# Optimization experiments

Hardware: AMD Instinct MI355X
Metric: run time of the kernel (lower is better)

Reference implementation:

```python
import jax, jax.numpy as jnp
import numpy as np

DIMS = 1024
HEAD = 16
HEAD_DIM = DIMS // HEAD
MAX_ITERS = 3
THRESH = 0.01   # torch uses self.threshold.item() -> plain float, no grad
FACTOR = 0.1    # torch uses self.factor.item()
EPS = 1e-5


def _ln(x, w):
    # LayerNorm(bias=False): (x-mean)/sqrt(var+eps) * w
    m = jnp.mean(x, axis=-1, keepdims=True)
    xc = x - m
    v = jnp.mean(xc * xc, axis=-1, keepdims=True)
    return xc * jax.lax.rsqrt(v + EPS) * w


def _focus(xw, Wq, bq, Wk, Wv, bv, Wo, bo, lna_w, lnb_w,
           lq_w, lq_b, lk_w, lk_b, lv_w, lv_b):
    # xw: [B, S, DIMS]. NOTE: in the torch code xa is effectively ignored inside
    # create_qkv (k/v are computed from x due to the `xa is not None` branch bug),
    # so each window is pure self-attention on the query window.
    B, S, D = xw.shape
    xn = _ln(xw, lna_w)
    scale = HEAD_DIM ** -0.25
    q = (xn @ Wq.T + bq) * scale
    k = (xn @ Wk.T) * scale          # k Linear has no bias
    v = xn @ Wv.T + bv

    def shp(t):
        return t.reshape(B, S, HEAD, HEAD_DIM).transpose(0, 2, 1, 3)  # [B,h,S,d]

    q, k, v = shp(q), shp(k), shp(v)
    q = _ln(q, lnb_w)
    k = _ln(k, lnb_w)

    causal = jnp.tril(jnp.ones((S, S), dtype=bool))
    neg = jnp.finfo(jnp.float32).min
    inv_sqrt_d = 1.0 / np.sqrt(HEAD_DIM).astype(np.float32)

    q_cur = q
    prev = jnp.zeros_like(q)
    attn_out = jnp.zeros_like(q)
    done = jnp.array(False)

    # eff_span == S here (span_len >= win_size, ctx % win_size == 0), so the
    # [:eff_span] slices in torch are no-ops. Unrolled loop with where-gating
    # reproduces the data-dependent early exit and stays reverse-differentiable.
    for it in range(MAX_ITERS):
        qp = _ln(q_cur @ lq_w.T + lq_b, lnb_w)
        kp = _ln(k @ lk_w.T + lk_b, lnb_w)
        vp = v @ lv_w.T + lv_b
        s = jnp.einsum('bhqd,bhkd->bhqk', qp, kp) * inv_sqrt_d
        s = jnp.where(causal, s, neg)
        a = jax.nn.softmax(s, axis=-1)
        o = jnp.einsum('bhqk,bhkd->bhqd', a, vp)
        # torch: permute(0,2,1,3).flatten(2) -> [B,S,h*d], then (buggy) raw
        # view(B, HEAD, S, HEAD_DIM) with NO transpose; out_proj is NOT applied
        # in this branch. Reproduced faithfully.
        iter_out = (o.transpose(0, 2, 1, 3)
                     .reshape(B, S, HEAD * HEAD_DIM)
                     .reshape(B, HEAD, S, HEAD_DIM))
        diff = jnp.mean(jnp.abs(iter_out - prev))
        conv = jnp.logical_and(diff < THRESH + FACTOR * diff, it > 0)
        attn_out = jnp.where(done, attn_out, iter_out)
        upd = jnp.logical_or(done, conv)
        q_cur = jnp.where(upd, q_cur, q_cur + iter_out)
        prev = jnp.where(upd, prev, iter_out)
        done = upd

    out = attn_out.transpose(0, 2, 1, 3).reshape(B, S, D)
    return out @ Wo.T + bo


def setup_inputs() -> dict:
    key = jax.random.key(0)
    ks = jax.random.split(key, 10)

    def w(k, shape, s=0.02):
        return jax.random.normal(k, shape, dtype=jnp.float32) * s

    return {
        'x': jax.random.normal(ks[0], (4, 4096, DIMS), dtype=jnp.float32),
        'Wq': w(ks[1], (DIMS, DIMS)), 'bq': jnp.zeros((DIMS,), jnp.float32),
        'Wk': w(ks[2], (DIMS, DIMS)),
        'Wv': w(ks[3], (DIMS, DIMS)), 'bv': jnp.zeros((DIMS,), jnp.float32),
        'Wo': w(ks[4], (DIMS, DIMS)), 'bo': jnp.zeros((DIMS,), jnp.float32),
        'lna_w': jnp.ones((DIMS,), jnp.float32),
        'lnb_w': jnp.ones((HEAD_DIM,), jnp.float32),
        'lq_w': w(ks[5], (HEAD_DIM, HEAD_DIM), 0.1), 'lq_b': jnp.zeros((HEAD_DIM,), jnp.float32),
        'lk_w': w(ks[6], (HEAD_DIM, HEAD_DIM), 0.1), 'lk_b': jnp.zeros((HEAD_DIM,), jnp.float32),
        'lv_w': w(ks[7], (HEAD_DIM, HEAD_DIM), 0.1), 'lv_b': jnp.zeros((HEAD_DIM,), jnp.float32),
        'win_size': 512,
        'span_len': 1024,
    }


def reference(x, Wq, bq, Wk, Wv, bv, Wo, bo, lna_w, lnb_w,
              lq_w, lq_b, lk_w, lk_b, lv_w, lv_b, win_size, span_len):
    # span_len only influences eff_span in torch; with span_len >= win_size it
    # has no effect on the math (k/v come from the query window due to the bug).
    b, ctx, dims = x.shape
    nwin = ctx // win_size  # ctx chosen divisible by win_size
    xw = x.reshape(b, nwin, win_size, dims).transpose(1, 0, 2, 3)  # [nwin,B,W,D]
    f = lambda xx: _focus(xx, Wq, bq, Wk, Wv, bv, Wo, bo, lna_w, lnb_w,
                          lq_w, lq_b, lk_w, lk_b, lv_w, lv_b)
    out = jax.vmap(f)(xw)  # per-window convergence test, matching torch
    return out.transpose(1, 0, 2, 3).reshape(b, ctx, dims)
```

## Files before the change

kernel.cpp:

```cpp
#include <hip/hip_runtime.h>
#include <math.h>

#define DIMS   1024
#define NHEAD  16
#define HD     64
#define WIN    512
#define CTX    4096
#define NBATCH 4
#define NROWS  (NBATCH*CTX)
#define NUNITS (NROWS*NHEAD)
#define LNEPS  1e-5f
#define FIXSCALE 16777216.0

typedef __attribute__((ext_vector_type(8))) short bf16x8;
typedef __attribute__((ext_vector_type(4))) float f32x4;

__device__ __forceinline__ float4 ld4(const float* p) { return *reinterpret_cast<const float4*>(p); }
__device__ __forceinline__ void st4(float* p, float4 v) { *reinterpret_cast<float4*>(p) = v; }

__device__ __forceinline__ float wave_sum64(float v) {
#pragma unroll
    for (int off = 32; off; off >>= 1) v += __shfl_xor(v, off, 64);
    return v;
}
__device__ __forceinline__ float grp16_sum(float v) {
    v += __shfl_xor(v, 1, 64);
    v += __shfl_xor(v, 2, 64);
    v += __shfl_xor(v, 4, 64);
    v += __shfl_xor(v, 8, 64);
    return v;
}

__device__ __forceinline__ unsigned bf16_rn_bits(float x) {
    unsigned u = __float_as_uint(x);
    return (u + 0x7fffu + ((u >> 16) & 1u)) >> 16;
}
__device__ __forceinline__ unsigned pack_hl(float x) {
    unsigned h = bf16_rn_bits(x);
    float hf = __uint_as_float(h << 16);
    unsigned l = bf16_rn_bits(x - hf);
    return (h << 16) | (l & 0xffffu);
}

__device__ __forceinline__ unsigned cvtpk_bf16(float a, float b) {
    unsigned r;
    asm volatile("v_cvt_pk_bf16_f32 %0, %1, %2" : "=v"(r) : "v"(a), "v"(b));
    return r;
}
__device__ __forceinline__ void split_pair(float a, float b, unsigned& hw, unsigned& lw) {
    hw = cvtpk_bf16(a, b);
    float ha = __uint_as_float(hw << 16);
    float hb = __uint_as_float(hw & 0xffff0000u);
    lw = cvtpk_bf16(a - ha, b - hb);
}

__device__ __forceinline__ int swzo(int row, int kbyte) {
    return ((row << 7) + kbyte) ^ ((row & 7) << 4);
}

__global__ __launch_bounds__(256)
void ln1024_pack_kernel(const float* __restrict__ x, const float* __restrict__ w,
                        unsigned* __restrict__ outp) {
    int r = blockIdx.x;
    int tid = threadIdx.x;
    const float* xr = x + (size_t)r * DIMS;
    float4 v = ld4(xr + (tid << 2));
    __shared__ float red[8];
    float s = wave_sum64(v.x + v.y + v.z + v.w);
    int wv = tid >> 6, lane = tid & 63;
    if (lane == 0) red[wv] = s;
    __syncthreads();
    float mean = (red[0] + red[1] + red[2] + red[3]) * (1.0f / DIMS);
    float dx = v.x - mean, dy = v.y - mean, dz = v.z - mean, dw = v.w - mean;
    float ss = wave_sum64(dx*dx + dy*dy + dz*dz + dw*dw);
    if (lane == 0) red[4 + wv] = ss;
    __syncthreads();
    float inv = rsqrtf((red[4] + red[5] + red[6] + red[7]) * (1.0f / DIMS) + LNEPS);
    float4 wv4 = ld4(w + (tid << 2));
    uint4 pk;
    pk.x = pack_hl(dx * inv * wv4.x);
    pk.y = pack_hl(dy * inv * wv4.y);
    pk.z = pack_hl(dz * inv * wv4.z);
    pk.w = pack_hl(dw * inv * wv4.w);
    *reinterpret_cast<uint4*>(outp + (size_t)r * DIMS + (tid << 2)) = pk;
}

template<int DO_HLN>
__global__ __launch_bounds__(256, 2)
void gemm_hl_kernel(const unsigned* __restrict__ Ahl, const float* __restrict__ W,
                    const float* __restrict__ bias, float* __restrict__ Cm,
                    float alpha, int has_bias, const float* __restrict__ lnw) {
    __shared__ short Ah[128 * 64], Al[128 * 64], Wh[128 * 64], Wl[128 * 64];
    int tid = threadIdx.x;
    int wid = tid >> 6, lane = tid & 63;
    int wm = (wid >> 1) << 6, wn = (wid & 1) << 6;
    int g4 = lane >> 4, l16 = lane & 15;
    int m0 = blockIdx.x << 7, n0 = blockIdx.y << 7;

    f32x4 acc[4][4] = {};

    int orow[4], okb[4];
#pragma unroll
    for (int j = 0; j < 4; ++j) {
        int oc = tid + (j << 8);
        orow[j] = oc >> 3;
        okb[j] = (oc & 7) << 4;
    }

    for (int k0 = 0; k0 < 1024; k0 += 64) {
        uint4 a0[4], a1[4];
        float4 w0[4], w1[4];
#pragma unroll
        for (int j = 0; j < 4; ++j) {
            const unsigned* ap = Ahl + (size_t)(m0 + orow[j]) * 1024 + k0 + (okb[j] >> 1);
            a0[j] = *reinterpret_cast<const uint4*>(ap);
            a1[j] = *reinterpret_cast<const uint4*>(ap + 4);
            const float* wp = W + (size_t)(n0 + orow[j]) * 1024 + k0 + (okb[j] >> 1);
            w0[j] = *reinterpret_cast<const float4*>(wp);
            w1[j] = *reinterpret_cast<const float4*>(wp + 4);
        }
        __syncthreads();
#pragma unroll
        for (int j = 0; j < 4; ++j) {
            int off = swzo(orow[j], okb[j]);
            uint4 hi, lo;
            hi.x = __byte_perm(a0[j].x, a0[j].y, 0x7632);
            hi.y = __byte_perm(a0[j].z, a0[j].w, 0x7632);
            hi.z = __byte_perm(a1[j].x, a1[j].y, 0x7632);
            hi.w = __byte_perm(a1[j].z, a1[j].w, 0x7632);
            lo.x = __byte_perm(a0[j].x, a0[j].y, 0x5410);
            lo.y = __byte_perm(a0[j].z, a0[j].w, 0x5410);
            lo.z = __byte_perm(a1[j].x, a1[j].y, 0x5410);
            lo.w = __byte_perm(a1[j].z, a1[j].w, 0x5410);
            *reinterpret_cast<uint4*>(reinterpret_cast<char*>(Ah) + off) = hi;
            *reinterpret_cast<uint4*>(reinterpret_cast<char*>(Al) + off) = lo;

            float xs[8];
            *reinterpret_cast<float4*>(&xs[0]) = w0[j];
            *reinterpret_cast<float4*>(&xs[4]) = w1[j];
            uint4 hw4, lw4;
            unsigned* hwp = &hw4.x;
            unsigned* lwp = &lw4.x;
#pragma unroll
            for (int p = 0; p < 4; ++p) {
                unsigned u0 = __float_as_uint(xs[2*p]);
                unsigned u1 = __float_as_uint(xs[2*p + 1]);
                unsigned h0 = (u0 + 0x8000u) >> 16;
                unsigned h1 = (u1 + 0x8000u) >> 16;
                float l0 = xs[2*p]     - __uint_as_float(h0 << 16);
                float l1 = xs[2*p + 1] - __uint_as_float(h1 << 16);
                unsigned lb0 = (__float_as_uint(l0) + 0x8000u) >> 16;
                unsigned lb1 = (__float_as_uint(l1) + 0x8000u) >> 16;
                hwp[p] = h0 | (h1 << 16);
                lwp[p] = lb0 | (lb1 << 16);
            }
            *reinterpret_cast<uint4*>(reinterpret_cast<char*>(Wh) + off) = hw4;
            *reinterpret_cast<uint4*>(reinterpret_cast<char*>(Wl) + off) = lw4;
        }
        __syncthreads();

#pragma unroll
        for (int kk = 0; kk < 2; ++kk) {
            bf16x8 afh[4], afl[4], wfh[4], wfl[4];
#pragma unroll
            for (int mt = 0; mt < 4; ++mt) {
                int row = wm + (mt << 4) + l16;
                int off = ((row << 7) + (kk << 6) + (g4 << 4)) ^ ((row & 7) << 4);
                afh[mt] = *reinterpret_cast<const bf16x8*>(reinterpret_cast<const char*>(Ah) + off);
                afl[mt] = *reinterpret_cast<const bf16x8*>(reinterpret_cast<const char*>(Al) + off);
            }
#pragma unroll
            for (int nt = 0; nt < 4; ++nt) {
                int row = wn + (nt << 4) + l16;
                int off = ((row << 7) + (kk << 6) + (g4 << 4)) ^ ((row & 7) << 4);
                wfh[nt] = *reinterpret_cast<const bf16x8*>(reinterpret_cast<const char*>(Wh) + off);
                wfl[nt] = *reinterpret_cast<const bf16x8*>(reinterpret_cast<const char*>(Wl) + off);
            }
#pragma unroll
            for (int mt = 0; mt < 4; ++mt)
#pragma unroll
                for (int nt = 0; nt < 4; ++nt) {
                    acc[mt][nt] = __builtin_amdgcn_mfma_f32_16x16x32_bf16(afh[mt], wfh[nt], acc[mt][nt], 0, 0, 0);
                    acc[mt][nt] = __builtin_amdgcn_mfma_f32_16x16x32_bf16(afl[mt], wfh[nt], acc[mt][nt], 0, 0, 0);
                    acc[mt][nt] = __builtin_amdgcn_mfma_f32_16x16x32_bf16(afh[mt], wfl[nt], acc[mt][nt], 0, 0, 0);
                }
        }
    }

    if (DO_HLN) {
        float bb[4];
#pragma unroll
        for (int nt = 0; nt < 4; ++nt)
            bb[nt] = has_bias ? bias[n0 + wn + (nt << 4) + l16] : 0.0f;
        float lw4[4];
#pragma unroll
        for (int nt = 0; nt < 4; ++nt) lw4[nt] = lnw[(nt << 4) + l16];
#pragma unroll
        for (int mt = 0; mt < 4; ++mt)
#pragma unroll
            for (int r = 0; r < 4; ++r) {
                float v[4];
                float s1 = 0.0f;
#pragma unroll
                for (int nt = 0; nt < 4; ++nt) {
                    v[nt] = alpha * (acc[mt][nt][r] + bb[nt]);
                    s1 += v[nt];
                }
                s1 = grp16_sum(s1);
                float mean = s1 * (1.0f / 64.0f);
                float s2 = 0.0f;
#pragma unroll
                for (int nt = 0; nt < 4; ++nt) { v[nt] -= mean; s2 += v[nt] * v[nt]; }
                s2 = grp16_sum(s2);
                float inv = rsqrtf(s2 * (1.0f / 64.0f) + LNEPS);
                int row = m0 + wm + (mt << 4) + (g4 << 2) + r;
#pragma unroll
                for (int nt = 0; nt < 4; ++nt)
                    Cm[(size_t)row * DIMS + n0 + wn + (nt << 4) + l16] = v[nt] * inv * lw4[nt];
            }
    } else {
#pragma unroll
        for (int mt = 0; mt < 4; ++mt)
#pragma unroll
            for (int nt = 0; nt < 4; ++nt) {
                int col = n0 + wn + (nt << 4) + l16;
                float bb = has_bias ? bias[col] : 0.0f;
#pragma unroll
                for (int r = 0; r < 4; ++r) {
                    int row = m0 + wm + (mt << 4) + (g4 << 2) + r;
                    Cm[(size_t)row * DIMS + col] = alpha * (acc[mt][nt][r] + bb);
                }
            }
    }
}

__global__ __launch_bounds__(256)
void proj64_khl_kernel(const float* __restrict__ inp, const float* __restrict__ W,
                       const float* __restrict__ Wb, const float* __restrict__ lnw,
                       unsigned* __restrict__ plane) {
    int u0 = blockIdx.x << 6;
    __shared__ float As[64][68];
    __shared__ float Bs[64][68];
    int tid = threadIdx.x;
    for (int e = tid; e < 4096; e += 256) Bs[e & 63][e >> 6] = W[e];
    for (int e = tid; e < 1024; e += 256) {
        int row = e >> 4;
        int col = (e & 15) << 2;
        float4 v = ld4(inp + ((size_t)(u0 + row) << 6) + col);
        As[col + 0][row] = v.x; As[col + 1][row] = v.y;
        As[col + 2][row] = v.z; As[col + 3][row] = v.w;
    }
    __syncthreads();
    int tm = tid >> 4, tn = tid & 15;
    float acc[4][4] = {};
#pragma unroll
    for (int k = 0; k < 64; ++k) {
        float4 av = ld4(&As[k][tm << 2]);
        float4 bv = ld4(&Bs[k][tn << 2]);
        float aa[4] = {av.x, av.y, av.z, av.w};
        float bb[4] = {bv.x, bv.y, bv.z, bv.w};
#pragma unroll
        for (int mm = 0; mm < 4; ++mm)
#pragma unroll
            for (int nn = 0; nn < 4; ++nn)
                acc[mm][nn] = fmaf(aa[mm], bb[nn], acc[mm][nn]);
    }
    float bb4[4] = {Wb[(tn << 2) + 0], Wb[(tn << 2) + 1], Wb[(tn << 2) + 2], Wb[(tn << 2) + 3]};
    float lw4[4] = {lnw[(tn << 2) + 0], lnw[(tn << 2) + 1], lnw[(tn << 2) + 2], lnw[(tn << 2) + 3]};
#pragma unroll
    for (int mm = 0; mm < 4; ++mm) {
        float o0 = acc[mm][0] + bb4[0], o1 = acc[mm][1] + bb4[1];
        float o2 = acc[mm][2] + bb4[2], o3 = acc[mm][3] + bb4[3];
        float mean = grp16_sum(o0 + o1 + o2 + o3) * (1.0f / 64.0f);
        float d0 = o0 - mean, d1 = o1 - mean, d2 = o2 - mean, d3 = o3 - mean;
        float var = grp16_sum(d0*d0 + d1*d1 + d2*d2 + d3*d3) * (1.0f / 64.0f);
        float inv = rsqrtf(var + LNEPS);
        o0 = d0 * inv * lw4[0]; o1 = d1 * inv * lw4[1];
        o2 = d2 * inv * lw4[2]; o3 = d3 * inv * lw4[3];
        int u_p = u0 + (tm << 2) + mm;
        int r = u_p >> 4, h = u_p & 15;
        int s = r & 511;
        int ua = ((r >> 9) << 4) + h;
        size_t punit = (size_t)ua * 512 + s;
        uint4 pk;
        pk.x = pack_hl(o0); pk.y = pack_hl(o1); pk.z = pack_hl(o2); pk.w = pack_hl(o3);
        *reinterpret_cast<uint4*>(plane + (punit << 6) + (tn << 2)) = pk;
    }
}

__global__ __launch_bounds__(256)
void proj64_vthl_kernel(const float* __restrict__ inp, const float* __restrict__ W,
                        const float* __restrict__ Wb, unsigned* __restrict__ plane) {
    int u0 = blockIdx.x << 6;
    __shared__ float As[64][68];
    __shared__ float Bs[64][68];
    int tid = threadIdx.x;
    for (int e = tid; e < 4096; e += 256) Bs[e & 63][e >> 6] = W[e];
    for (int e = tid; e < 1024; e += 256) {
        int row = e >> 4;
        int col = (e & 15) << 2;
        float4 v = ld4(inp + ((size_t)(u0 + row) << 6) + col);
        As[col + 0][row] = v.x; As[col + 1][row] = v.y;
        As[col + 2][row] = v.z; As[col + 3][row] = v.w;
    }
    __syncthreads();
    int tm = tid >> 4, tn = tid & 15;
    float acc[4][4] = {};
#pragma unroll
    for (int k = 0; k < 64; ++k) {
        float4 av = ld4(&As[k][tm << 2]);
        float4 bv = ld4(&Bs[k][tn << 2]);
        float aa[4] = {av.x, av.y, av.z, av.w};
        float bb[4] = {bv.x, bv.y, bv.z, bv.w};
#pragma unroll
        for (int mm = 0; mm < 4; ++mm)
#pragma unroll
            for (int nn = 0; nn < 4; ++nn)
                acc[mm][nn] = fmaf(aa[mm], bb[nn], acc[mm][nn]);
    }
    float bb4[4] = {Wb[(tn << 2) + 0], Wb[(tn << 2) + 1], Wb[(tn << 2) + 2], Wb[(tn << 2) + 3]};
#pragma unroll
    for (int mm = 0; mm < 4; ++mm) {
        int u_p = u0 + (tm << 2) + mm;
        int r = u_p >> 4, h = u_p & 15;
        int s = r & 511;
        int ua = ((r >> 9) << 4) + h;
        size_t base = ((size_t)(ua * 8 + (s >> 6)) << 12) + (s & 63);
#pragma unroll
        for (int nn = 0; nn < 4; ++nn) {
            int d = (tn << 2) + nn;
            plane[base + ((size_t)d << 6)] = pack_hl(acc[mm][nn] + bb4[nn]);
        }
    }
}

template<int DIFF, int USE_CONV>
__global__ __launch_bounds__(256)
void attn_mfma_kernel(const float* __restrict__ qacc, const unsigned* __restrict__ khl,
                      const unsigned* __restrict__ vthl, float* __restrict__ o_io,
                      const float* __restrict__ lqw, const float* __restrict__ lqb,
                      const float* __restrict__ lnw,
                      unsigned long long* __restrict__ diff_acc,
                      const int* __restrict__ conv) {
    __shared__ short kh[64][72], kl[64][72], vh[64][72], vl[64][72];
    __shared__ float dred[4];

    int blk = blockIdx.x;
    int u = blk & 511;
    int pr = blk >> 9;
    int tHi = 7 - (pr << 1);
    int tLo = tHi - 1;
    int h = u & 15;
    int w = (u >> 4) & 7;
    int b = u >> 7;
    if (USE_CONV && conv[w]) return;
    int rowbase = b * CTX + w * WIN;
    int col0 = h * HD;
    int tid = threadIdx.x;
    int wv = tid >> 6;
    int lane = tid & 63;
    int g4 = lane >> 4;
    int qcol = lane & 15;
    int q_loc = (wv << 4) + qcol;
    int selhi = g4 >> 1;

    const unsigned* kbase = khl + (((size_t)u * 512) << 6);
    const unsigned* vbase = vthl + (((size_t)u * 8) << 12);

    uint4 kpre[4], vpre[4];
#pragma unroll
    for (int rr = 0; rr < 4; ++rr) {
        int row = (wv << 4) + (rr << 2) + g4;
        kpre[rr] = *reinterpret_cast<const uint4*>(kbase + ((size_t)row << 6) + (qcol << 2));
        vpre[rr] = *reinterpret_cast<const uint4*>(vbase + ((size_t)row << 6) + (qcol << 2));
    }

#pragma unroll
    for (int rr = 0; rr < 4; ++rr) {
        int row = (wv << 4) + (rr << 2) + g4;
        float4 v = ld4(lqw + (row << 6) + (qcol << 2));
        unsigned h0, l0, h1, l1;
        split_pair(v.x, v.y, h0, l0);
        split_pair(v.z, v.w, h1, l1);
        *reinterpret_cast<uint2*>(&kh[row][qcol << 2]) = make_uint2(h0, h1);
        *reinterpret_cast<uint2*>(&kl[row][qcol << 2]) = make_uint2(l0, l1);
    }
    __syncthreads();

    bf16x8 qfh[2][2], qfl[2][2];
#pragma unroll
    for (int ti = 0; ti < 2; ++ti) {
        int T = ti ? tLo : tHi;
        bf16x8 bqh[2], bql[2];
        {
            const float* qrow = qacc + (size_t)(rowbase + (T << 6) + q_loc) * DIMS + col0;
#pragma unroll
            for (int kb = 0; kb < 2; ++kb) {
                float4 x0 = ld4(qrow + (kb << 5) + (g4 << 3));
                float4 x1 = ld4(qrow + (kb << 5) + (g4 << 3) + 4);
                unsigned hws[4], lws[4];
                split_pair(x0.x, x0.y, hws[0], lws[0]);
                split_pair(x0.z, x0.w, hws[1], lws[1]);
                split_pair(x1.x, x1.y, hws[2], lws[2]);
                split_pair(x1.z, x1.w, hws[3], lws[3]);
#pragma unroll
                for (int p2 = 0; p2 < 4; ++p2) {
                    reinterpret_cast<unsigned*>(&bqh[kb])[p2] = hws[p2];
                    reinterpret_cast<unsigned*>(&bql[kb])[p2] = lws[p2];
                }
            }
        }
        f32x4 qpa[4] = {{0,0,0,0},{0,0,0,0},{0,0,0,0},{0,0,0,0}};
        __builtin_amdgcn_s_setprio(1);
#pragma unroll
        for (int jt = 0; jt < 4; ++jt) {
// ... 170 lines not shown
                        unsigned lB = __shfl(lwp[(kb2 << 2) + 2 + (ip & 1)], srcl, 64);
                        reinterpret_cast<unsigned*>(&ph)[ip] = selhi ? hB : hA;
                        reinterpret_cast<unsigned*>(&pl)[ip] = selhi ? lB : lA;
                    }
#pragma unroll
                    for (int dt = 0; dt < 4; ++dt) {
                        int drow = (dt << 4) + qcol;
                        bf16x8 ah = *reinterpret_cast<const bf16x8*>(&vh[drow][(kb2 << 5) + (g4 << 3)]);
                        bf16x8 al = *reinterpret_cast<const bf16x8*>(&vl[drow][(kb2 << 5) + (g4 << 3)]);
                        oacc[ti][dt] = __builtin_amdgcn_mfma_f32_16x16x32_bf16(ah, ph, oacc[ti][dt], 0, 0, 0);
                        oacc[ti][dt] = __builtin_amdgcn_mfma_f32_16x16x32_bf16(al, ph, oacc[ti][dt], 0, 0, 0);
                        oacc[ti][dt] = __builtin_amdgcn_mfma_f32_16x16x32_bf16(ah, pl, oacc[ti][dt], 0, 0, 0);
                    }
                }
                __builtin_amdgcn_s_setprio(0);
            }
        }
        __syncthreads();
    }

    float dsum = 0.0f;
#pragma unroll
    for (int ti = 0; ti < 2; ++ti) {
        int T = ti ? tLo : tHi;
        float invl = 1.0f / l_r[ti];
        float* orow = o_io + (size_t)(rowbase + (T << 6) + q_loc) * DIMS + col0;
#pragma unroll
        for (int dt = 0; dt < 4; ++dt) {
            float4 ov = make_float4(oacc[ti][dt][0] * invl, oacc[ti][dt][1] * invl,
                                    oacc[ti][dt][2] * invl, oacc[ti][dt][3] * invl);
            float* addr = orow + (dt << 4) + (g4 << 2);
            if (DIFF) {
                float4 pv4 = ld4(addr);
                dsum += fabsf(ov.x - pv4.x) + fabsf(ov.y - pv4.y)
                      + fabsf(ov.z - pv4.z) + fabsf(ov.w - pv4.w);
            }
            st4(addr, ov);
        }
    }
    if (DIFF) {
        float s = wave_sum64(dsum);
        if (lane == 0) dred[wv] = s;
        __syncthreads();
        if (tid == 0) {
            double tot = (double)(dred[0] + dred[1] + dred[2] + dred[3]);
            unsigned long long q = (unsigned long long)(tot * FIXSCALE + 0.5);
            atomicAdd(&diff_acc[w], q);
        }
    }
}

__global__ __launch_bounds__(256)
void scatter_add_kernel(float* __restrict__ qacc, const float* __restrict__ o) {
    size_t gid = (size_t)blockIdx.x * 256 + threadIdx.x;
    size_t flat = gid << 2;
    int uu = (int)(flat >> 6);
    int col = (int)(flat & 63);
    int r = uu >> 4, h = uu & 15;
    int s = r & 511;
    int rb = r - s;
    size_t src = ((size_t)(rb + h * 32 + (s >> 4)) << 10)
               + (size_t)((s & 15) << 6) + col;
    float4 a = ld4(qacc + flat);
    float4 bv = ld4(o + src);
    st4(qacc + flat, make_float4(a.x + bv.x, a.y + bv.y, a.z + bv.z, a.w + bv.w));
}

__global__ void init_ctrl_kernel(unsigned long long* __restrict__ dacc,
                                 int* __restrict__ conv) {
    int i = threadIdx.x;
    if (i < 8) { dacc[i] = 0ULL; conv[i] = 0; }
}

__global__ void conv_from_acc_kernel(const unsigned long long* __restrict__ dacc,
                                     int* __restrict__ conv) {
    int w = threadIdx.x;
    if (w < 8) {
        float mean = (float)((double)dacc[w] * (1.0 / (FIXSCALE * 2097152.0)));
        conv[w] = (mean < 0.01f + 0.1f * mean) ? 1 : 0;
    }
}

__global__ __launch_bounds__(256)
void unscramble_pack_kernel(const float* __restrict__ src, unsigned* __restrict__ outp) {
    size_t gid = (size_t)blockIdx.x * 256 + threadIdx.x;
    size_t flat = gid << 2;
    int r = (int)(flat >> 10);
    int e = (int)(flat & 1023);
    int h2 = e >> 6, d2 = e & 63;
    int s2 = r & 511;
    int rb = r - s2;
    size_t sidx = ((size_t)(rb + h2 * 32 + (s2 >> 4)) << 10) + (size_t)((s2 & 15) << 6) + d2;
    float4 v = ld4(src + sidx);
    uint4 pk;
    pk.x = pack_hl(v.x); pk.y = pack_hl(v.y); pk.z = pack_hl(v.z); pk.w = pack_hl(v.w);
    *reinterpret_cast<uint4*>(outp + flat) = pk;
}

extern "C" void kernel_launch(void* const* d_in, const int* in_sizes, int n_in,
                              void* d_out, int out_size, void* d_ws, size_t ws_size,
                              hipStream_t stream) {
    (void)in_sizes; (void)n_in; (void)out_size; (void)ws_size;
    const float* x   = (const float*)d_in[0];
    const float* Wq  = (const float*)d_in[1];
    const float* bq  = (const float*)d_in[2];
    const float* Wk  = (const float*)d_in[3];
    const float* Wv  = (const float*)d_in[4];
    const float* bv  = (const float*)d_in[5];
    const float* Wo  = (const float*)d_in[6];
    const float* bo  = (const float*)d_in[7];
    const float* lna = (const float*)d_in[8];
    const float* lnb = (const float*)d_in[9];
    const float* lqw = (const float*)d_in[10];
    const float* lqb = (const float*)d_in[11];
    const float* lkw = (const float*)d_in[12];
    const float* lkb = (const float*)d_in[13];
    const float* lvw = (const float*)d_in[14];
    const float* lvb = (const float*)d_in[15];

    const size_t BUF = (size_t)NROWS * DIMS;
    unsigned long long* dacc = (unsigned long long*)d_ws;
    int* conv = (int*)(dacc + 8);
    float* R1 = (float*)((char*)d_ws + 4096);
    float* R2 = R1 + BUF;
    float* R3 = R2 + BUF;
    float* E  = (float*)d_out;

    const float scale = 0.35355339059327373f;

    ln1024_pack_kernel<<<NROWS, 256, 0, stream>>>(x, lna, (unsigned*)R2);

    dim3 gg(NROWS / 128, DIMS / 128);
    gemm_hl_kernel<1><<<gg, 256, 0, stream>>>((const unsigned*)R2, Wq, bq, R1, scale, 1, lnb);
    gemm_hl_kernel<1><<<gg, 256, 0, stream>>>((const unsigned*)R2, Wk, bq, E,  scale, 0, lnb);
    gemm_hl_kernel<0><<<gg, 256, 0, stream>>>((const unsigned*)R2, Wv, bv, R3, 1.0f, 1, lnb);

    proj64_khl_kernel<<<NUNITS / 64, 256, 0, stream>>>(E, lkw, lkb, lnb, (unsigned*)R2);
    proj64_vthl_kernel<<<NUNITS / 64, 256, 0, stream>>>(R3, lvw, lvb, (unsigned*)E);

    init_ctrl_kernel<<<1, 64, 0, stream>>>(dacc, conv);

    const unsigned* KHL = (const unsigned*)R2;
    const unsigned* VTHL = (const unsigned*)E;

    attn_mfma_kernel<0, 0><<<512 * 4, 256, 0, stream>>>(R1, KHL, VTHL, R3, lqw, lqb, lnb, dacc, conv);
    scatter_add_kernel<<<NROWS * DIMS / 4 / 256, 256, 0, stream>>>(R1, R3);
    attn_mfma_kernel<1, 0><<<512 * 4, 256, 0, stream>>>(R1, KHL, VTHL, R3, lqw, lqb, lnb, dacc, conv);
    conv_from_acc_kernel<<<1, 64, 0, stream>>>(dacc, conv);
    scatter_add_kernel<<<NROWS * DIMS / 4 / 256, 256, 0, stream>>>(R1, R3);
    attn_mfma_kernel<0, 1><<<512 * 4, 256, 0, stream>>>(R1, KHL, VTHL, R3, lqw, lqb, lnb, dacc, conv);

    unscramble_pack_kernel<<<NROWS * DIMS / 4 / 256, 256, 0, stream>>>(R3, (unsigned*)R2);
    gemm_hl_kernel<0><<<gg, 256, 0, stream>>>((const unsigned*)R2, Wo, bo, (float*)d_out, 1.0f, 1, lnb);
}
```

Before: 1.018 ms.

## Fuse per-head K/V 64x64 projections into the K and V GEMM epilogues

The K and V GEMMs now run the per-head 64x64 projection (lk/lv) in their epilogues. Each wave stages its 64x64 output tile in shared memory reused via a union, multiplies it by the split bf16 hi/lo projection weights with MFMA, and writes the packed K and transposed V planes directly. This removes two separate FP32 SIMT projection kernels and the full-size float round trip through global memory between them. The cost is extra epilogue work, more registers in the GEMM, and reshuffled workspace buffers.

Measured after the change: 1.165 ms. 1.14x slower.

```diff
diff --git a/kernel.cpp b/kernel.cpp
--- a/kernel.cpp
+++ b/kernel.cpp
@@ -85,12 +85,17 @@
     *reinterpret_cast<uint4*>(outp + (size_t)r * DIMS + (tid << 2)) = pk;
 }
 
-template<int DO_HLN>
+template<int EPI>
 __global__ __launch_bounds__(256, 2)
 void gemm_hl_kernel(const unsigned* __restrict__ Ahl, const float* __restrict__ W,
                     const float* __restrict__ bias, float* __restrict__ Cm,
-                    float alpha, int has_bias, const float* __restrict__ lnw) {
-    __shared__ short Ah[128 * 64], Al[128 * 64], Wh[128 * 64], Wl[128 * 64];
+                    unsigned* __restrict__ plane, float alpha, int has_bias,
+                    const float* __restrict__ lnw, const float* __restrict__ pw,
+                    const float* __restrict__ pb) {
+    __shared__ union {
+        struct { short Ah[8192], Al[8192], Wh[8192], Wl[8192]; } m;
+        unsigned kp[4][64][68];
+    } sm;
     int tid = threadIdx.x;
     int wid = tid >> 6, lane = tid & 63;
     int wm = (wid >> 1) << 6, wn = (wid & 1) << 6;
@@ -132,8 +137,8 @@
             lo.y = __byte_perm(a0[j].z, a0[j].w, 0x5410);
             lo.z = __byte_perm(a1[j].x, a1[j].y, 0x5410);
             lo.w = __byte_perm(a1[j].z, a1[j].w, 0x5410);
-            *reinterpret_cast<uint4*>(reinterpret_cast<char*>(Ah) + off) = hi;
-            *reinterpret_cast<uint4*>(reinterpret_cast<char*>(Al) + off) = lo;
+            *reinterpret_cast<uint4*>(reinterpret_cast<char*>(sm.m.Ah) + off) = hi;
+            *reinterpret_cast<uint4*>(reinterpret_cast<char*>(sm.m.Al) + off) = lo;
 
             float xs[8];
             *reinterpret_cast<float4*>(&xs[0]) = w0[j];
@@ -142,20 +147,9 @@
             unsigned* hwp = &hw4.x;
             unsigned* lwp = &lw4.x;
 #pragma unroll
-            for (int p = 0; p < 4; ++p) {
-                unsigned u0 = __float_as_uint(xs[2*p]);
-                unsigned u1 = __float_as_uint(xs[2*p + 1]);
-                unsigned h0 = (u0 + 0x8000u) >> 16;
-                unsigned h1 = (u1 + 0x8000u) >> 16;
-                float l0 = xs[2*p]     - __uint_as_float(h0 << 16);
-                float l1 = xs[2*p + 1] - __uint_as_float(h1 << 16);
-                unsigned lb0 = (__float_as_uint(l0) + 0x8000u) >> 16;
-                unsigned lb1 = (__float_as_uint(l1) + 0x8000u) >> 16;
-                hwp[p] = h0 | (h1 << 16);
-                lwp[p] = lb0 | (lb1 << 16);
-            }
-            *reinterpret_cast<uint4*>(reinterpret_cast<char*>(Wh) + off) = hw4;
-            *reinterpret_cast<uint4*>(reinterpret_cast<char*>(Wl) + off) = lw4;
+            for (int p = 0; p < 4; ++p) split_pair(xs[2*p], xs[2*p + 1], hwp[p], lwp[p]);
+            *reinterpret_cast<uint4*>(reinterpret_cast<char*>(sm.m.Wh) + off) = hw4;
+            *reinterpret_cast<uint4*>(reinterpret_cast<char*>(sm.m.Wl) + off) = lw4;
         }
         __syncthreads();
 
@@ -166,15 +160,15 @@
             for (int mt = 0; mt < 4; ++mt) {
                 int row = wm + (mt << 4) + l16;
                 int off = ((row << 7) + (kk << 6) + (g4 << 4)) ^ ((row & 7) << 4);
-                afh[mt] = *reinterpret_cast<const bf16x8*>(reinterpret_cast<const char*>(Ah) + off);
-                afl[mt] = *reinterpret_cast<const bf16x8*>(reinterpret_cast<const char*>(Al) + off);
+                afh[mt] = *reinterpret_cast<const bf16x8*>(reinterpret_cast<const char*>(sm.m.Ah) + off);
+                afl[mt] = *reinterpret_cast<const bf16x8*>(reinterpret_cast<const char*>(sm.m.Al) + off);
             }
 #pragma unroll
             for (int nt = 0; nt < 4; ++nt) {
                 int row = wn + (nt << 4) + l16;
                 int off = ((row << 7) + (kk << 6) + (g4 << 4)) ^ ((row & 7) << 4);
-                wfh[nt] = *reinterpret_cast<const bf16x8*>(reinterpret_cast<const char*>(Wh) + off);
-                wfl[nt] = *reinterpret_cast<const bf16x8*>(reinterpret_cast<const char*>(Wl) + off);
+                wfh[nt] = *reinterpret_cast<const bf16x8*>(reinterpret_cast<const char*>(sm.m.Wh) + off);
+                wfl[nt] = *reinterpret_cast<const bf16x8*>(reinterpret_cast<const char*>(sm.m.Wl) + off);
             }
 #pragma unroll
             for (int mt = 0; mt < 4; ++mt)
@@ -187,7 +181,137 @@
         }
     }
 
-    if (DO_HLN) {
+    if (EPI >= 2) {
+        __syncthreads();
+        int head = (n0 + wn) >> 6;
+        int rowbase0 = m0 + wm;
+
+        if (EPI == 2) {
+            float lw4[4];
+#pragma unroll
+            for (int nt = 0; nt < 4; ++nt) lw4[nt] = lnw[(nt << 4) + l16];
+#pragma unroll
+            for (int mt = 0; mt < 4; ++mt)
+#pragma unroll
+                for (int r = 0; r < 4; ++r) {
+                    float v[4];
+                    float s1 = 0.0f;
+#pragma unroll
+                    for (int nt = 0; nt < 4; ++nt) { v[nt] = alpha * acc[mt][nt][r]; s1 += v[nt]; }
+                    s1 = grp16_sum(s1);
+                    float mean = s1 * (1.0f / 64.0f);
+                    float s2 = 0.0f;
+#pragma unroll
+                    for (int nt = 0; nt < 4; ++nt) { v[nt] -= mean; s2 += v[nt] * v[nt]; }
+                    s2 = grp16_sum(s2);
+                    float inv = rsqrtf(s2 * (1.0f / 64.0f) + LNEPS);
+                    int row = (mt << 4) + (g4 << 2) + r;
+#pragma unroll
+                    for (int nt = 0; nt < 4; ++nt)
+                        sm.kp[wid][row][(nt << 4) + l16] = pack_hl(v[nt] * inv * lw4[nt]);
+                }
+        } else {
+            float bb[4];
+#pragma unroll
+            for (int nt = 0; nt < 4; ++nt)
+                bb[nt] = has_bias ? bias[n0 + wn + (nt << 4) + l16] : 0.0f;
+#pragma unroll
+            for (int mt = 0; mt < 4; ++mt)
+#pragma unroll
+                for (int r = 0; r < 4; ++r) {
+                    int row = (mt << 4) + (g4 << 2) + r;
+#pragma unroll
+                    for (int nt = 0; nt < 4; ++nt)
+                        sm.kp[wid][row][(nt << 4) + l16] = pack_hl(alpha * (acc[mt][nt][r] + bb[nt]));
+                }
+        }
+
+        bf16x8 pwh[4][2], pwl[4][2];
+        float pbv[4], lnww[4];
+#pragma unroll
+        for (int dg = 0; dg < 4; ++dg) {
+            pbv[dg] = pb[(dg << 4) + l16];
+            if (EPI == 2) lnww[dg] = lnw[(dg << 4) + l16];
+#pragma unroll
+            for (int kb = 0; kb < 2; ++kb) {
+                const float* wrow = pw + (((dg << 4) + l16) << 6) + (kb << 5) + (g4 << 3);
+                float4 x0 = ld4(wrow);
+                float4 x1 = ld4(wrow + 4);
+                unsigned hws[4], lws[4];
+                split_pair(x0.x, x0.y, hws[0], lws[0]);
+                split_pair(x0.z, x0.w, hws[1], lws[1]);
+                split_pair(x1.x, x1.y, hws[2], lws[2]);
+                split_pair(x1.z, x1.w, hws[3], lws[3]);
+#pragma unroll
+                for (int p2 = 0; p2 < 4; ++p2) {
+                    reinterpret_cast<unsigned*>(&pwh[dg][kb])[p2] = hws[p2];
+                    reinterpret_cast<unsigned*>(&pwl[dg][kb])[p2] = lws[p2];
+                }
+            }
+        }
+
+#pragma unroll
+        for (int rg = 0; rg < 4; ++rg) {
+            bf16x8 ahf[2], alf[2];
+#pragma unroll
+            for (int kb = 0; kb < 2; ++kb) {
+                const unsigned* kr = &sm.kp[wid][(rg << 4) + l16][(kb << 5) + (g4 << 3)];
+                uint4 p0 = *reinterpret_cast<const uint4*>(kr);
+                uint4 p1 = *reinterpret_cast<const uint4*>(kr + 4);
+                reinterpret_cast<unsigned*>(&ahf[kb])[0] = __byte_perm(p0.x, p0.y, 0x7632);
+                reinterpret_cast<unsigned*>(&ahf[kb])[1] = __byte_perm(p0.z, p0.w, 0x7632);
+                reinterpret_cast<unsigned*>(&ahf[kb])[2] = __byte_perm(p1.x, p1.y, 0x7632);
+                reinterpret_cast<unsigned*>(&ahf[kb])[3] = __byte_perm(p1.z, p1.w, 0x7632);
+                reinterpret_cast<unsigned*>(&alf[kb])[0] = __byte_perm(p0.x, p0.y, 0x5410);
+                reinterpret_cast<unsigned*>(&alf[kb])[1] = __byte_perm(p0.z, p0.w, 0x5410);
+                reinterpret_cast<unsigned*>(&alf[kb])[2] = __byte_perm(p1.x, p1.y, 0x5410);
+                reinterpret_cast<unsigned*>(&alf[kb])[3] = __byte_perm(p1.z, p1.w, 0x5410);
+            }
+            f32x4 pacc[4] = {{0,0,0,0},{0,0,0,0},{0,0,0,0},{0,0,0,0}};
+#pragma unroll
+            for (int kb = 0; kb < 2; ++kb)
+#pragma unroll
+                for (int dg = 0; dg < 4; ++dg) {
+                    pacc[dg] = __builtin_amdgcn_mfma_f32_16x16x32_bf16(ahf[kb], pwh[dg][kb], pacc[dg], 0, 0, 0);
+                    pacc[dg] = __builtin_amdgcn_mfma_f32_16x16x32_bf16(alf[kb], pwh[dg][kb], pacc[dg], 0, 0, 0);
+                    pacc[dg] = __builtin_amdgcn_mfma_f32_16x16x32_bf16(ahf[kb], pwl[dg][kb], pacc[dg], 0, 0, 0);
+                }
+            if (EPI == 2) {
+#pragma unroll
+                for (int r = 0; r < 4; ++r) {
+                    float vv[4];
+                    float s1 = 0.0f;
+#pragma unroll
+                    for (int dg = 0; dg < 4; ++dg) { vv[dg] = pacc[dg][r] + pbv[dg]; s1 += vv[dg]; }
+                    s1 = grp16_sum(s1);
+                    float mean = s1 * (1.0f / 64.0f);
+                    float s2 = 0.0f;
+#pragma unroll
+                    for (int dg = 0; dg < 4; ++dg) { vv[dg] -= mean; s2 += vv[dg] * vv[dg]; }
+                    s2 = grp16_sum(s2);
+                    float inv = rsqrtf(s2 * (1.0f / 64.0f) + LNEPS);
+                    int grow = rowbase0 + (rg << 4) + (g4 << 2) + r;
+                    int s = grow & 511;
+                    int ua = ((grow >> 9) << 4) + head;
+                    size_t punit = (size_t)ua * 512 + s;
+#pragma unroll
+                    for (int dg = 0; dg < 4; ++dg)
+                        plane[(punit << 6) + (dg << 4) + l16] = pack_hl(vv[dg] * inv * lnww[dg]);
+                }
+            } else {
+#pragma unroll
+                for (int r = 0; r < 4; ++r) {
+                    int grow = rowbase0 + (rg << 4) + (g4 << 2) + r;
+                    int s = grow & 511;
+                    int ua = ((grow >> 9) << 4) + head;
+                    size_t base = ((size_t)(ua * 8 + (s >> 6)) << 12) + (s & 63);
+#pragma unroll
+                    for (int dg = 0; dg < 4; ++dg)
+                        plane[base + ((size_t)((dg << 4) + l16) << 6)] = pack_hl(pacc[dg][r] + pbv[dg]);
+                }
+            }
+        }
+    } else if (EPI == 1) {
         float bb[4];
 #pragma unroll
         for (int nt = 0; nt < 4; ++nt)
@@ -231,106 +355,6 @@
                     Cm[(size_t)row * DIMS + col] = alpha * (acc[mt][nt][r] + bb);
                 }
             }
-    }
-}
-
-__global__ __launch_bounds__(256)
-void proj64_khl_kernel(const float* __restrict__ inp, const float* __restrict__ W,
-                       const float* __restrict__ Wb, const float* __restrict__ lnw,
-                       unsigned* __restrict__ plane) {
-    int u0 = blockIdx.x << 6;
-    __shared__ float As[64][68];
-    __shared__ float Bs[64][68];
-    int tid = threadIdx.x;
-    for (int e = tid; e < 4096; e += 256) Bs[e & 63][e >> 6] = W[e];
-    for (int e = tid; e < 1024; e += 256) {
-        int row = e >> 4;
-        int col = (e & 15) << 2;
-        float4 v = ld4(inp + ((size_t)(u0 + row) << 6) + col);
-        As[col + 0][row] = v.x; As[col + 1][row] = v.y;
-        As[col + 2][row] = v.z; As[col + 3][row] = v.w;
-    }
-    __syncthreads();
-    int tm = tid >> 4, tn = tid & 15;
-    float acc[4][4] = {};
-#pragma unroll
-    for (int k = 0; k < 64; ++k) {
-        float4 av = ld4(&As[k][tm << 2]);
-        float4 bv = ld4(&Bs[k][tn << 2]);
-        float aa[4] = {av.x, av.y, av.z, av.w};
-        float bb[4] = {bv.x, bv.y, bv.z, bv.w};
-#pragma unroll
-        for (int mm = 0; mm < 4; ++mm)
-#pragma unroll
-            for (int nn = 0; nn < 4; ++nn)
-                acc[mm][nn] = fmaf(aa[mm], bb[nn], acc[mm][nn]);
-    }
-    float bb4[4] = {Wb[(tn << 2) + 0], Wb[(tn << 2) + 1], Wb[(tn << 2) + 2], Wb[(tn << 2) + 3]};
-    float lw4[4] = {lnw[(tn << 2) + 0], lnw[(tn << 2) + 1], lnw[(tn << 2) + 2], lnw[(tn << 2) + 3]};
-#pragma unroll
-    for (int mm = 0; mm < 4; ++mm) {
-        float o0 = acc[mm][0] + bb4[0], o1 = acc[mm][1] + bb4[1];
-        float o2 = acc[mm][2] + bb4[2], o3 = acc[mm][3] + bb4[3];
-        float mean = grp16_sum(o0 + o1 + o2 + o3) * (1.0f / 64.0f);
-        float d0 = o0 - mean, d1 = o1 - mean, d2 = o2 - mean, d3 = o3 - mean;
-        float var = grp16_sum(d0*d0 + d1*d1 + d2*d2 + d3*d3) * (1.0f / 64.0f);
-        float inv = rsqrtf(var + LNEPS);
-        o0 = d0 * inv * lw4[0]; o1 = d1 * inv * lw4[1];
-        o2 = d2 * inv * lw4[2]; o3 = d3 * inv * lw4[3];
-        int u_p = u0 + (tm << 2) + mm;
-        int r = u_p >> 4, h = u_p & 15;
-        int s = r & 511;
-        int ua = ((r >> 9) << 4) + h;
-        size_t punit = (size_t)ua * 512 + s;
-        uint4 pk;
-        pk.x = pack_hl(o0); pk.y = pack_hl(o1); pk.z = pack_hl(o2); pk.w = pack_hl(o3);
-        *reinterpret_cast<uint4*>(plane + (punit << 6) + (tn << 2)) = pk;
-    }
-}
-
-__global__ __launch_bounds__(256)
-void proj64_vthl_kernel(const float* __restrict__ inp, const float* __restrict__ W,
-                        const float* __restrict__ Wb, unsigned* __restrict__ plane) {
-    int u0 = blockIdx.x << 6;
-    __shared__ float As[64][68];
-    __shared__ float Bs[64][68];
-    int tid = threadIdx.x;
-    for (int e = tid; e < 4096; e += 256) Bs[e & 63][e >> 6] = W[e];
-    for (int e = tid; e < 1024; e += 256) {
-        int row = e >> 4;
-        int col = (e & 15) << 2;
-        float4 v = ld4(inp + ((size_t)(u0 + row) << 6) + col);
-        As[col + 0][row] = v.x; As[col + 1][row] = v.y;
-        As[col + 2][row] = v.z; As[col + 3][row] = v.w;
-    }
-    __syncthreads();
-    int tm = tid >> 4, tn = tid & 15;
-    float acc[4][4] = {};
-#pragma unroll
-    for (int k = 0; k < 64; ++k) {
-        float4 av = ld4(&As[k][tm << 2]);
-        float4 bv = ld4(&Bs[k][tn << 2]);
-        float aa[4] = {av.x, av.y, av.z, av.w};
-        float bb[4] = {bv.x, bv.y, bv.z, bv.w};
-#pragma unroll
-        for (int mm = 0; mm < 4; ++mm)
-#pragma unroll
-            for (int nn = 0; nn < 4; ++nn)
-                acc[mm][nn] = fmaf(aa[mm], bb[nn], acc[mm][nn]);
-    }
-    float bb4[4] = {Wb[(tn << 2) + 0], Wb[(tn << 2) + 1], Wb[(tn << 2) + 2], Wb[(tn << 2) + 3]};
-#pragma unroll
-    for (int mm = 0; mm < 4; ++mm) {
-        int u_p = u0 + (tm << 2) + mm;
-        int r = u_p >> 4, h = u_p & 15;
-        int s = r & 511;
-        int ua = ((r >> 9) << 4) + h;
-        size_t base = ((size_t)(ua * 8 + (s >> 6)) << 12) + (s & 63);
-#pragma unroll
-        for (int nn = 0; nn < 4; ++nn) {
-            int d = (tn << 2) + nn;
-            plane[base + ((size_t)d << 6)] = pack_hl(acc[mm][nn] + bb4[nn]);
-        }
     }
 }
 
@@ -716,25 +740,26 @@
     ln1024_pack_kernel<<<NROWS, 256, 0, stream>>>(x, lna, (unsigned*)R2);
 
     dim3 gg(NROWS / 128, DIMS / 128);
-    gemm_hl_kernel<1><<<gg, 256, 0, stream>>>((const unsigned*)R2, Wq, bq, R1, scale, 1, lnb);
-    gemm_hl_kernel<1><<<gg, 256, 0, stream>>>((const unsigned*)R2, Wk, bq, E,  scale, 0, lnb);
-    gemm_hl_kernel<0><<<gg, 256, 0, stream>>>((const unsigned*)R2, Wv, bv, R3, 1.0f, 1, lnb);
-
-    proj64_khl_kernel<<<NUNITS / 64, 256, 0, stream>>>(E, lkw, lkb, lnb, (unsigned*)R2);
-    proj64_vthl_kernel<<<NUNITS / 64, 256, 0, stream>>>(R3, lvw, lvb, (unsigned*)E);
+    gemm_hl_kernel<1><<<gg, 256, 0, stream>>>((const unsigned*)R2, Wq, bq, R1, nullptr,
+                                              scale, 1, lnb, lqw, lqb);
+    gemm_hl_kernel<2><<<gg, 256, 0, stream>>>((const unsigned*)R2, Wk, bq, nullptr, (unsigned*)E,
+                                              scale, 0, lnb, lkw, lkb);
+    gemm_hl_kernel<3><<<gg, 256, 0, stream>>>((const unsigned*)R2, Wv, bv, nullptr, (unsigned*)R3,
+                                              1.0f, 1, lnb, lvw, lvb);
 
     init_ctrl_kernel<<<1, 64, 0, stream>>>(dacc, conv);
 
-    const unsigned* KHL = (const unsigned*)R2;
-    const unsigned* VTHL = (const unsigned*)E;
-
-    attn_mfma_kernel<0, 0><<<512 * 4, 256, 0, stream>>>(R1, KHL, VTHL, R3, lqw, lqb, lnb, dacc, conv);
-    scatter_add_kernel<<<NROWS * DIMS / 4 / 256, 256, 0, stream>>>(R1, R3);
-    attn_mfma_kernel<1, 0><<<512 * 4, 256, 0, stream>>>(R1, KHL, VTHL, R3, lqw, lqb, lnb, dacc, conv);
+    const unsigned* KHL = (const unsigned*)E;
+    const unsigned* VTHL = (const unsigned*)R3;
+
+    attn_mfma_kernel<0, 0><<<512 * 4, 256, 0, stream>>>(R1, KHL, VTHL, R2, lqw, lqb, lnb, dacc, conv);
+    scatter_add_kernel<<<NROWS * DIMS / 4 / 256, 256, 0, stream>>>(R1, R2);
+    attn_mfma_kernel<1, 0><<<512 * 4, 256, 0, stream>>>(R1, KHL, VTHL, R2, lqw, lqb, lnb, dacc, conv);
     conv_from_acc_kernel<<<1, 64, 0, stream>>>(dacc, conv);
-    scatter_add_kernel<<<NROWS * DIMS / 4 / 256, 256, 0, stream>>>(R1, R3);
-    attn_mfma_kernel<0, 1><<<512 * 4, 256, 0, stream>>>(R1, KHL, VTHL, R3, lqw, lqb, lnb, dacc, conv);
-
-    unscramble_pack_kernel<<<NROWS * DIMS / 4 / 256, 256, 0, stream>>>(R3, (unsigned*)R2);
-    gemm_hl_kernel<0><<<gg, 256, 0, stream>>>((const unsigned*)R2, Wo, bo, (float*)d_out, 1.0f, 1, lnb);
-}
+    scatter_add_kernel<<<NROWS * DIMS / 4 / 256, 256, 0, stream>>>(R1, R2);
+    attn_mfma_kernel<0, 1><<<512 * 4, 256, 0, stream>>>(R1, KHL, VTHL, R2, lqw, lqb, lnb, dacc, conv);
+
+    unscramble_pack_kernel<<<NROWS * DIMS / 4 / 256, 256, 0, stream>>>(R2, (unsigned*)R3);
+    gemm_hl_kernel<0><<<gg, 256, 0, stream>>>((const unsigned*)R3, Wo, bo, (float*)d_out, nullptr,
+                                              1.0f, 1, lnb, lqw, lqb);
+}
```

## Store activations as separate hi/lo bf16 planes and pre-split weights for GEMMs

Applied to the files above, without the earlier changes.

Changes the LayerNorm and unscramble kernels to write separate hi and lo bf16 planes instead of interleaved packed words, so the GEMM stages them into shared memory with direct copies and no byte permutes. Weights for Q, K and O are pre-split into hi/lo bf16 arrays by a separate kernel, which removes the per-tile float-to-bf16 split work inside the GEMM. The V GEMM still splits its weights inline, using the hardware pack-convert instruction in place of manual rounding. This adds extra small kernel launches and a few MB of weight-split traffic, and it reuses scratch buffers, which depends on their lifetimes not overlapping.

Measured after the change: 1.457 ms. +43.2%, slower.

```diff
diff --git a/kernel.cpp b/kernel.cpp
--- a/kernel.cpp
+++ b/kernel.cpp
@@ -59,8 +59,8 @@
 }
 
 __global__ __launch_bounds__(256)
-void ln1024_pack_kernel(const float* __restrict__ x, const float* __restrict__ w,
-                        unsigned* __restrict__ outp) {
+void ln1024_split_kernel(const float* __restrict__ x, const float* __restrict__ w,
+                         unsigned short* __restrict__ hp, unsigned short* __restrict__ lp) {
     int r = blockIdx.x;
     int tid = threadIdx.x;
     const float* xr = x + (size_t)r * DIMS;
@@ -77,17 +77,32 @@
     __syncthreads();
     float inv = rsqrtf((red[4] + red[5] + red[6] + red[7]) * (1.0f / DIMS) + LNEPS);
     float4 wv4 = ld4(w + (tid << 2));
-    uint4 pk;
-    pk.x = pack_hl(dx * inv * wv4.x);
-    pk.y = pack_hl(dy * inv * wv4.y);
-    pk.z = pack_hl(dz * inv * wv4.z);
-    pk.w = pack_hl(dw * inv * wv4.w);
-    *reinterpret_cast<uint4*>(outp + (size_t)r * DIMS + (tid << 2)) = pk;
-}
-
-template<int DO_HLN>
+    unsigned h0, l0, h1, l1;
+    split_pair(dx * inv * wv4.x, dy * inv * wv4.y, h0, l0);
+    split_pair(dz * inv * wv4.z, dw * inv * wv4.w, h1, l1);
+    size_t base = (size_t)r * DIMS + (tid << 2);
+    *reinterpret_cast<uint2*>(hp + base) = make_uint2(h0, h1);
+    *reinterpret_cast<uint2*>(lp + base) = make_uint2(l0, l1);
+}
+
+__global__ __launch_bounds__(256)
+void presplit_w_kernel(const float* __restrict__ W, unsigned short* __restrict__ hp,
+                       unsigned short* __restrict__ lp) {
+    size_t gid = (size_t)blockIdx.x * 256 + threadIdx.x;
+    size_t base = gid << 2;
+    float4 v = ld4(W + base);
+    unsigned h0, l0, h1, l1;
+    split_pair(v.x, v.y, h0, l0);
+    split_pair(v.z, v.w, h1, l1);
+    *reinterpret_cast<uint2*>(hp + base) = make_uint2(h0, h1);
+    *reinterpret_cast<uint2*>(lp + base) = make_uint2(l0, l1);
+}
+
+template<int DO_HLN, int PREW>
 __global__ __launch_bounds__(256, 2)
-void gemm_hl_kernel(const unsigned* __restrict__ Ahl, const float* __restrict__ W,
+void gemm_hl_kernel(const unsigned short* __restrict__ Ahp, const unsigned short* __restrict__ Alp,
+                    const float* __restrict__ Wf,
+                    const unsigned short* __restrict__ Whp, const unsigned short* __restrict__ Wlp,
                     const float* __restrict__ bias, float* __restrict__ Cm,
                     float alpha, int has_bias, const float* __restrict__ lnw) {
     __shared__ short Ah[128 * 64], Al[128 * 64], Wh[128 * 64], Wl[128 * 64];
@@ -108,54 +123,36 @@
     }
 
     for (int k0 = 0; k0 < 1024; k0 += 64) {
-        uint4 a0[4], a1[4];
-        float4 w0[4], w1[4];
+        uint4 ah4[4], al4[4], wh4[4], wl4[4];
+        float4 wf0[4], wf1[4];
 #pragma unroll
         for (int j = 0; j < 4; ++j) {
-            const unsigned* ap = Ahl + (size_t)(m0 + orow[j]) * 1024 + k0 + (okb[j] >> 1);
-            a0[j] = *reinterpret_cast<const uint4*>(ap);
-            a1[j] = *reinterpret_cast<const uint4*>(ap + 4);
-            const float* wp = W + (size_t)(n0 + orow[j]) * 1024 + k0 + (okb[j] >> 1);
-            w0[j] = *reinterpret_cast<const float4*>(wp);
-            w1[j] = *reinterpret_cast<const float4*>(wp + 4);
+            size_t abase = (size_t)(m0 + orow[j]) * 1024 + k0 + (okb[j] >> 1);
+            ah4[j] = *reinterpret_cast<const uint4*>(Ahp + abase);
+            al4[j] = *reinterpret_cast<const uint4*>(Alp + abase);
+            size_t wbase = (size_t)(n0 + orow[j]) * 1024 + k0 + (okb[j] >> 1);
+            if (PREW) {
+                wh4[j] = *reinterpret_cast<const uint4*>(Whp + wbase);
+                wl4[j] = *reinterpret_cast<const uint4*>(Wlp + wbase);
+            } else {
+                wf0[j] = ld4(Wf + wbase);
+                wf1[j] = ld4(Wf + wbase + 4);
+            }
         }
         __syncthreads();
 #pragma unroll
         for (int j = 0; j < 4; ++j) {
             int off = swzo(orow[j], okb[j]);
-            uint4 hi, lo;
-            hi.x = __byte_perm(a0[j].x, a0[j].y, 0x7632);
-            hi.y = __byte_perm(a0[j].z, a0[j].w, 0x7632);
-            hi.z = __byte_perm(a1[j].x, a1[j].y, 0x7632);
-            hi.w = __byte_perm(a1[j].z, a1[j].w, 0x7632);
-            lo.x = __byte_perm(a0[j].x, a0[j].y, 0x5410);
-            lo.y = __byte_perm(a0[j].z, a0[j].w, 0x5410);
-            lo.z = __byte_perm(a1[j].x, a1[j].y, 0x5410);
-            lo.w = __byte_perm(a1[j].z, a1[j].w, 0x5410);
-            *reinterpret_cast<uint4*>(reinterpret_cast<char*>(Ah) + off) = hi;
-            *reinterpret_cast<uint4*>(reinterpret_cast<char*>(Al) + off) = lo;
-
-            float xs[8];
-            *reinterpret_cast<float4*>(&xs[0]) = w0[j];
-            *reinterpret_cast<float4*>(&xs[4]) = w1[j];
-            uint4 hw4, lw4;
-            unsigned* hwp = &hw4.x;
-            unsigned* lwp = &lw4.x;
-#pragma unroll
-            for (int p = 0; p < 4; ++p) {
-                unsigned u0 = __float_as_uint(xs[2*p]);
-                unsigned u1 = __float_as_uint(xs[2*p + 1]);
-                unsigned h0 = (u0 + 0x8000u) >> 16;
-                unsigned h1 = (u1 + 0x8000u) >> 16;
-                float l0 = xs[2*p]     - __uint_as_float(h0 << 16);
-                float l1 = xs[2*p + 1] - __uint_as_float(h1 << 16);
-                unsigned lb0 = (__float_as_uint(l0) + 0x8000u) >> 16;
-                unsigned lb1 = (__float_as_uint(l1) + 0x8000u) >> 16;
-                hwp[p] = h0 | (h1 << 16);
-                lwp[p] = lb0 | (lb1 << 16);
-            }
-            *reinterpret_cast<uint4*>(reinterpret_cast<char*>(Wh) + off) = hw4;
-            *reinterpret_cast<uint4*>(reinterpret_cast<char*>(Wl) + off) = lw4;
+            *reinterpret_cast<uint4*>(reinterpret_cast<char*>(Ah) + off) = ah4[j];
+            *reinterpret_cast<uint4*>(reinterpret_cast<char*>(Al) + off) = al4[j];
+            if (!PREW) {
+                split_pair(wf0[j].x, wf0[j].y, wh4[j].x, wl4[j].x);
+                split_pair(wf0[j].z, wf0[j].w, wh4[j].y, wl4[j].y);
+                split_pair(wf1[j].x, wf1[j].y, wh4[j].z, wl4[j].z);
+                split_pair(wf1[j].z, wf1[j].w, wh4[j].w, wl4[j].w);
+            }
+            *reinterpret_cast<uint4*>(reinterpret_cast<char*>(Wh) + off) = wh4[j];
+            *reinterpret_cast<uint4*>(reinterpret_cast<char*>(Wl) + off) = wl4[j];
         }
         __syncthreads();
 
@@ -667,7 +664,8 @@
 }
 
 __global__ __launch_bounds__(256)
-void unscramble_pack_kernel(const float* __restrict__ src, unsigned* __restrict__ outp) {
+void unscramble_split_kernel(const float* __restrict__ src, unsigned short* __restrict__ hp,
+                             unsigned short* __restrict__ lp) {
     size_t gid = (size_t)blockIdx.x * 256 + threadIdx.x;
     size_t flat = gid << 2;
     int r = (int)(flat >> 10);
@@ -677,9 +675,11 @@
     int rb = r - s2;
     size_t sidx = ((size_t)(rb + h2 * 32 + (s2 >> 4)) << 10) + (size_t)((s2 & 15) << 6) + d2;
     float4 v = ld4(src + sidx);
-    uint4 pk;
-    pk.x = pack_hl(v.x); pk.y = pack_hl(v.y); pk.z = pack_hl(v.z); pk.w = pack_hl(v.w);
-    *reinterpret_cast<uint4*>(outp + flat) = pk;
+    unsigned h0, l0, h1, l1;
+    split_pair(v.x, v.y, h0, l0);
+    split_pair(v.z, v.w, h1, l1);
+    *reinterpret_cast<uint2*>(hp + flat) = make_uint2(h0, h1);
+    *reinterpret_cast<uint2*>(lp + flat) = make_uint2(l0, l1);
 }
 
 extern "C" void kernel_launch(void* const* d_in, const int* in_sizes, int n_in,
@@ -711,14 +711,26 @@
     float* R3 = R2 + BUF;
     float* E  = (float*)d_out;
 
+    unsigned short* XNH = (unsigned short*)R2;
+    unsigned short* XNL = XNH + BUF;
+    unsigned short* WSH = (unsigned short*)R3;
+    unsigned short* WSL = WSH + (size_t)DIMS * DIMS;
+    unsigned short* WOH = (unsigned short*)R1;
+    unsigned short* WOL = WOH + (size_t)DIMS * DIMS;
+    unsigned short* PH  = (unsigned short*)R2;
+    unsigned short* PL  = PH + BUF;
+
     const float scale = 0.35355339059327373f;
-
-    ln1024_pack_kernel<<<NROWS, 256, 0, stream>>>(x, lna, (unsigned*)R2);
+    const int WGRID = DIMS * DIMS / 4 / 256;
+
+    ln1024_split_kernel<<<NROWS, 256, 0, stream>>>(x, lna, XNH, XNL);
 
     dim3 gg(NROWS / 128, DIMS / 128);
-    gemm_hl_kernel<1><<<gg, 256, 0, stream>>>((const unsigned*)R2, Wq, bq, R1, scale, 1, lnb);
-    gemm_hl_kernel<1><<<gg, 256, 0, stream>>>((const unsigned*)R2, Wk, bq, E,  scale, 0, lnb);
-    gemm_hl_kernel<0><<<gg, 256, 0, stream>>>((const unsigned*)R2, Wv, bv, R3, 1.0f, 1, lnb);
+    presplit_w_kernel<<<WGRID, 256, 0, stream>>>(Wq, WSH, WSL);
+    gemm_hl_kernel<1, 1><<<gg, 256, 0, stream>>>(XNH, XNL, nullptr, WSH, WSL, bq, R1, scale, 1, lnb);
+    presplit_w_kernel<<<WGRID, 256, 0, stream>>>(Wk, WSH, WSL);
+    gemm_hl_kernel<1, 1><<<gg, 256, 0, stream>>>(XNH, XNL, nullptr, WSH, WSL, bq, E, scale, 0, lnb);
+    gemm_hl_kernel<0, 0><<<gg, 256, 0, stream>>>(XNH, XNL, Wv, nullptr, nullptr, bv, R3, 1.0f, 1, lnb);
 
     proj64_khl_kernel<<<NUNITS / 64, 256, 0, stream>>>(E, lkw, lkb, lnb, (unsigned*)R2);
     proj64_vthl_kernel<<<NUNITS / 64, 256, 0, stream>>>(R3, lvw, lvb, (unsigned*)E);
@@ -735,6 +747,7 @@
     scatter_add_kernel<<<NROWS * DIMS / 4 / 256, 256, 0, stream>>>(R1, R3);
     attn_mfma_kernel<0, 1><<<512 * 4, 256, 0, stream>>>(R1, KHL, VTHL, R3, lqw, lqb, lnb, dacc, conv);
 
-    unscramble_pack_kernel<<<NROWS * DIMS / 4 / 256, 256, 0, stream>>>(R3, (unsigned*)R2);
-    gemm_hl_kernel<0><<<gg, 256, 0, stream>>>((const unsigned*)R2, Wo, bo, (float*)d_out, 1.0f, 1, lnb);
-}
+    unscramble_split_kernel<<<NROWS * DIMS / 4 / 256, 256, 0, stream>>>(R3, PH, PL);
+    presplit_w_kernel<<<WGRID, 256, 0, stream>>>(Wo, WOH, WOL);
+    gemm_hl_kernel<0, 1><<<gg, 256, 0, stream>>>(PH, PL, nullptr, WOH, WOL, bo, (float*)d_out, 1.0f, 1, lnb);
+}
```
